# Performance work log

Hardware: AMD Instinct MI355X
Metric: run time of the kernel (lower is better)

The kernel has to match this reference:

```python
import jax, jax.numpy as jnp
import numpy as np

WASHOUT = 200  # matches init kwarg


def setup_inputs() -> dict:
    key = jax.random.key(0)
    k1, k2, k3, k4 = jax.random.split(key, 4)
    N = 4096  # hidden_nodes
    T = 4096  # timeseries length
    density = 0.2  # w_res_density
    u = jax.random.normal(k1, (T,), dtype=jnp.float32)
    # sparse reservoir matrix scaled to spectral radius 0.9
    w_res = jax.random.uniform(k2, (N, N), dtype=jnp.float32) - 0.5
    keep = jax.random.uniform(k3, (N, N)) <= density
    w_res = jnp.where(keep, w_res, 0.0)
    eigs = np.linalg.eigvals(np.asarray(w_res, dtype=np.float64))
    w_res = w_res * jnp.float32(0.9 / np.max(np.abs(eigs)))
    w_in = jax.random.uniform(k4, (N,), dtype=jnp.float32) - 0.5  # uniform distrib, density 1.0, scaling 1.0
    w_out = jnp.ones((N,), dtype=jnp.float32)
    # w_out_density = 1.0 -> mask is a random permutation of all N node indices
    w_out_mask = jax.random.permutation(jax.random.fold_in(key, 7), N).astype(jnp.int32)
    return {"u": u, "w_res": w_res, "w_in": w_in, "w_out": w_out, "w_out_mask": w_out_mask}


def reference(u, w_res, w_in, w_out, w_out_mask):
    N = w_res.shape[0]
    x0 = jnp.zeros((N,), dtype=u.dtype)

    def step(x, u_t):
        x = jnp.tanh(w_in * u_t + w_res @ x)  # [N]
        return x, x[w_out_mask]  # collect masked (permuted) state

    _, X = jax.lax.scan(step, x0, u)  # X: [T, N]
    X = X[WASHOUT:]
    return X @ w_out  # [T - washout]
```

## Files before the change

kernel.cpp:

```cpp
#include <hip/hip_runtime.h>
#include <hip/hip_runtime_api.h>
#include <hip/hip_fp16.h>
#include <math.h>


#define Nn 4096
#define WASHOUT_N 200
#define NBLOCKS 256
#define TPB 1024
#define ROWS_PER_BLOCK 16
#define NWAVES 16
#define ELL_CAP 1024

typedef unsigned long long u64t;
typedef unsigned int u32t;

static __device__ __forceinline__ unsigned short f2h(float f) {
    __half h = __float2half_rn(f);
    union { __half h; unsigned short u; } cv; cv.h = h; return cv.u;
}
static __device__ __forceinline__ float h2f(unsigned short ub) {
    union { __half h; unsigned short u; } cv; cv.u = ub; return __half2float(cv.h);
}

__global__ __launch_bounds__(256) void esn_init(
    const float* __restrict__ w_out, const int* __restrict__ mask,
    u32t* __restrict__ xp_a, u32t* __restrict__ xp_b,
    float* __restrict__ w_eff, float* __restrict__ out, int out_n)
{
    int i = blockIdx.x * blockDim.x + threadIdx.x;
    if (i < Nn) {
        xp_a[i] = 0u;
        xp_b[i] = 0xFFFF0000u;
        w_eff[mask[i]] = w_out[i];
        if (i < out_n) out[i] = 0.0f;
    }
}

__global__ __launch_bounds__(256) void build_ell(
    const float* __restrict__ W, float* __restrict__ ev,
    unsigned short* __restrict__ ec)
{
    int row = blockIdx.x;
    __shared__ unsigned int bank_cnt[32];
    __shared__ unsigned int group_cnt[16];
    if (threadIdx.x < 32) bank_cnt[threadIdx.x] = 0u;
    if (threadIdx.x < 16) group_cnt[threadIdx.x] = 0u;
    __syncthreads();

    const float* wr = W + (size_t)row * Nn;
    size_t base = (size_t)row * ELL_CAP;

    for (int s = threadIdx.x; s < ELL_CAP; s += 256) {
        ev[base + s] = 0.0f;
        ec[base + s] = 0;
    }
    __syncthreads();

    for (int j = threadIdx.x; j < Nn; j += 256) {
        float v = wr[j];
        if (v != 0.0f) {
            unsigned int b  = (unsigned int)j & 31u;
            unsigned int jb = atomicAdd(&bank_cnt[b], 1u);
            unsigned int g  = jb & 15u;
            unsigned int s  = 0xFFFFFFFFu;
            for (int tries = 0; tries < 16; ++tries) {
                unsigned int cand = atomicAdd(&group_cnt[g], 1u);
                if (cand < 64u) { s = cand; break; }
                g = (g + 1u) & 15u;
            }
            if (s != 0xFFFFFFFFu) {
                unsigned int i = g >> 2, k = g & 3u;
                unsigned int pos = 4u * (i * 64u + s) + k;
                ev[base + pos] = v;
                ec[base + pos] = (unsigned short)j;
            }
        }
    }
}

__device__ __forceinline__ u64t xload64(const u64t* p) {
    return __hip_atomic_load(p, __ATOMIC_RELAXED, __HIP_MEMORY_SCOPE_AGENT);
}

__global__ __launch_bounds__(TPB) void esn_step_sparse(
    const float* __restrict__ u, const float* __restrict__ w_in,
    const float* __restrict__ ev, const unsigned short* __restrict__ ec,
    u32t* xp_a, u32t* xp_b, const float* __restrict__ w_eff,
    unsigned short* __restrict__ hist, float* __restrict__ out, int T)
{
    __shared__ __align__(16) float xs[Nn];
    __shared__ u32t  xpub[NWAVES];
    __shared__ float dpart[NWAVES];

    const int tid  = threadIdx.x;
    const int lane = tid & 63;
    const int wave = tid >> 6;
    const int base_row = blockIdx.x * ROWS_PER_BLOCK;
    const int row  = base_row + wave;

    const float wi = w_in[row];
    const float we0 = w_eff[tid];
    const float we1 = w_eff[TPB + tid];
    const float we2 = w_eff[2 * TPB + tid];
    const float we3 = w_eff[3 * TPB + tid];

    const float4*  v4 = (const float4*)(ev + (size_t)row * ELL_CAP);
    const ushort4* c4 = (const ushort4*)(ec + (size_t)row * ELL_CAP);
    const float4  rv0 = v4[lane],       rv1 = v4[64 + lane],
                  rv2 = v4[128 + lane], rv3 = v4[192 + lane];
    const ushort4 rc0 = c4[lane],       rc1 = c4[64 + lane],
                  rc2 = c4[128 + lane], rc3 = c4[192 + lane];

    u32t* bufs[2] = { xp_a, xp_b };
    const bool have_hist = (hist != nullptr);

    for (int t = 0; t <= T; ++t) {
        if (t == T && have_hist) break;

        u32t* xc = bufs[t & 1];
        const u64t tg = (u64t)(u32t)t;
        const float ut = (t < T) ? u[t] : 0.0f;

        const u64t* p = (const u64t*)xc + 2 * tid;
        u64t a = xload64(p);
        u64t b = xload64(p + 1);
        for (;;) {
            bool okA = (((a >> 16) & 0xFFFFull) == tg) && ((a >> 48) == tg);
            bool okB = (((b >> 16) & 0xFFFFull) == tg) && ((b >> 48) == tg);
            if (okA && okB) break;
            __builtin_amdgcn_s_sleep(1);
            if (!okA) a = xload64(p);
            if (!okB) b = xload64(p + 1);
        }
        ((float4*)xs)[tid] = make_float4(
            h2f((unsigned short)(a & 0xFFFF)),
            h2f((unsigned short)((a >> 32) & 0xFFFF)),
            h2f((unsigned short)(b & 0xFFFF)),
            h2f((unsigned short)((b >> 32) & 0xFFFF)));
        __syncthreads();

        if (t < T) {
            float acc = 0.0f;
            acc += rv0.x * xs[rc0.x]; acc += rv0.y * xs[rc0.y];
            acc += rv0.z * xs[rc0.z]; acc += rv0.w * xs[rc0.w];
            acc += rv1.x * xs[rc1.x]; acc += rv1.y * xs[rc1.y];
            acc += rv1.z * xs[rc1.z]; acc += rv1.w * xs[rc1.w];
            acc += rv2.x * xs[rc2.x]; acc += rv2.y * xs[rc2.y];
            acc += rv2.z * xs[rc2.z]; acc += rv2.w * xs[rc2.w];
            acc += rv3.x * xs[rc3.x]; acc += rv3.y * xs[rc3.y];
            acc += rv3.z * xs[rc3.z]; acc += rv3.w * xs[rc3.w];
            #pragma unroll
            for (int off = 32; off > 0; off >>= 1)
                acc += __shfl_xor(acc, off, 64);

            if (lane == 0) {
                float z = __fmaf_rn(wi, ut, acc);
                float e = __expf(2.0f * z);
                float xnew = 1.0f - 2.0f / (e + 1.0f);
                xpub[wave] = ((u32t)(t + 1) << 16) | (u32t)f2h(xnew);
            }
        }

        const bool des = (!have_hist) && (t >= WASHOUT_N + 1) &&
                         ((t & (NBLOCKS - 1)) == (int)blockIdx.x);
        if (des) {
            float d = we0 * xs[tid] + we1 * xs[TPB + tid]
                    + we2 * xs[2 * TPB + tid] + we3 * xs[3 * TPB + tid];
            #pragma unroll
            for (int off = 32; off > 0; off >>= 1)
                d += __shfl_xor(d, off, 64);
            if (lane == 0) dpart[wave] = d;
        }
        __syncthreads();

        if (wave == 0) {
            if (t < T && lane < ROWS_PER_BLOCK) {
                u32t w = xpub[lane];
                __hip_atomic_store(&bufs[(t + 1) & 1][base_row + lane], w,
                                   __ATOMIC_RELAXED, __HIP_MEMORY_SCOPE_AGENT);
                if (have_hist)
                    hist[(size_t)t * Nn + base_row + lane] =
                        (unsigned short)(w & 0xFFFF);
            }
            if (des) {
                float s = (lane < NWAVES) ? dpart[lane] : 0.0f;
                #pragma unroll
                for (int off = 8; off > 0; off >>= 1)
                    s += __shfl_xor(s, off, 64);
                if (lane == 0) out[t - WASHOUT_N - 1] = s;
            }
        }
    }
}

__global__ __launch_bounds__(256) void esn_out_gemv(
    const unsigned short* __restrict__ hist, const float* __restrict__ w_eff,
    float* __restrict__ out, int n_out)
{
    __shared__ float swave[4];
    int k = blockIdx.x;
    if (k >= n_out) return;
    const __half2* hp = (const __half2*)(hist + (size_t)(k + WASHOUT_N) * Nn);
    const int tid = threadIdx.x;
    float acc = 0.0f;
    #pragma unroll
    for (int j = tid; j < Nn / 2; j += 256) {
        float2 xv = __half22float2(hp[j]);
        acc += w_eff[2 * j] * xv.x + w_eff[2 * j + 1] * xv.y;
    }
    #pragma unroll
    for (int off = 32; off > 0; off >>= 1)
        acc += __shfl_xor(acc, off, 64);
    if ((tid & 63) == 0) swave[tid >> 6] = acc;
    __syncthreads();
    if (tid == 0) out[k] = swave[0] + swave[1] + swave[2] + swave[3];
}

extern "C" void kernel_launch(void* const* d_in, const int* in_sizes, int n_in,
                              void* d_out, int out_size, void* d_ws, size_t ws_size,
                              hipStream_t stream)
{
    const float* u     = (const float*)d_in[0];
    const float* W     = (const float*)d_in[1];
    const float* w_in  = (const float*)d_in[2];
    const float* w_out = (const float*)d_in[3];
    const int*   mask  = (const int*)d_in[4];
    float* out = (float*)d_out;
    int T = in_sizes[0];

    const size_t ev_bytes   = (size_t)Nn * ELL_CAP * sizeof(float);
    const size_t ec_bytes   = (size_t)Nn * ELL_CAP * sizeof(unsigned short);
    const size_t hist_bytes = (size_t)Nn * Nn * sizeof(unsigned short);
    const size_t aux_bytes  = 64 * 1024;
    char* ws = (char*)d_ws;

    const bool fits_hist = ws_size >= ev_bytes + ec_bytes + hist_bytes + aux_bytes;
    const bool fits_ell  = ws_size >= ev_bytes + ec_bytes + aux_bytes;

    if (fits_ell) {
        size_t off = ev_bytes + ec_bytes;
        float*          ev    = (float*)(ws);
        unsigned short* ec    = (unsigned short*)(ws + ev_bytes);
        unsigned short* hist  = fits_hist ? (unsigned short*)(ws + off) : nullptr;
        if (fits_hist) off += hist_bytes;
        u32t*           xp_a  = (u32t*)(ws + off);
        u32t*           xp_b  = (u32t*)(ws + off + 16384);
        float*          w_eff = (float*)(ws + off + 32768);

        hipLaunchKernelGGL(esn_init, dim3(16), dim3(256), 0, stream,
                           w_out, mask, xp_a, xp_b, w_eff, out, out_size);
        hipLaunchKernelGGL(build_ell, dim3(Nn), dim3(256), 0, stream, W, ev, ec);

        void* args[] = { (void*)&u, (void*)&w_in, (void*)&ev, (void*)&ec,
                         (void*)&xp_a, (void*)&xp_b, (void*)&w_eff,
                         (void*)&hist, (void*)&out, (void*)&T };
        hipError_t err = hipLaunchCooperativeKernel((const void*)esn_step_sparse,
                                                    dim3(NBLOCKS), dim3(TPB),
                                                    args, 0, stream);
        if (err != hipSuccess) {
            hipLaunchKernelGGL(esn_step_sparse, dim3(NBLOCKS), dim3(TPB), 0, stream,
                               u, w_in, ev, ec, xp_a, xp_b, w_eff, hist, out, T);
        }
        if (fits_hist) {
            hipLaunchKernelGGL(esn_out_gemv, dim3(out_size), dim3(256), 0, stream,
                               hist, w_eff, out, out_size);
        }
    }
}
```

Before: 9.762 ms.

## Double-buffer shared state, publish per wave, trim ELL groups, use DPP reductions

Shared state is double-buffered so the second block-wide barrier per timestep can be removed. Each wave now publishes its own row directly after a DPP-based reduction instead of staging it through shared memory. The ELL builder counts nonzeros per row and packs them into only as many 64-entry groups as needed, so the step kernel can skip unused gather slots. The spin-wait also polls a few times before sleeping. The gains come with more complex synchronisation, and barriers are still taken inside the rarely-true output branch.

```diff
diff --git a/kernel.cpp b/kernel.cpp
--- a/kernel.cpp
+++ b/kernel.cpp
@@ -23,6 +23,10 @@
     union { __half h; unsigned short u; } cv; cv.u = ub; return __half2float(cv.h);
 }
 
+#define DPP_ADD(x, ctrl, rmask)                                              \
+    x += __int_as_float(__builtin_amdgcn_update_dpp(                         \
+        0, __float_as_int(x), (ctrl), (rmask), 0xf, true))
+
 __global__ __launch_bounds__(256) void esn_init(
     const float* __restrict__ w_out, const int* __restrict__ mask,
     u32t* __restrict__ xp_a, u32t* __restrict__ xp_b,
@@ -39,35 +43,47 @@
 
 __global__ __launch_bounds__(256) void build_ell(
     const float* __restrict__ W, float* __restrict__ ev,
-    unsigned short* __restrict__ ec)
+    unsigned short* __restrict__ ec, int* __restrict__ gcnt)
 {
     int row = blockIdx.x;
     __shared__ unsigned int bank_cnt[32];
     __shared__ unsigned int group_cnt[16];
+    __shared__ unsigned int nnz_cnt;
     if (threadIdx.x < 32) bank_cnt[threadIdx.x] = 0u;
     if (threadIdx.x < 16) group_cnt[threadIdx.x] = 0u;
+    if (threadIdx.x == 0) nnz_cnt = 0u;
     __syncthreads();
 
     const float* wr = W + (size_t)row * Nn;
     size_t base = (size_t)row * ELL_CAP;
+
+    unsigned int mycnt = 0;
+    for (int j = threadIdx.x; j < Nn; j += 256)
+        if (wr[j] != 0.0f) ++mycnt;
+    atomicAdd(&nnz_cnt, mycnt);
 
     for (int s = threadIdx.x; s < ELL_CAP; s += 256) {
         ev[base + s] = 0.0f;
         ec[base + s] = 0;
     }
     __syncthreads();
+
+    unsigned int G = (nnz_cnt + 63u) / 64u;
+    if (G < 1u) G = 1u;
+    if (G > 16u) G = 16u;
+    if (threadIdx.x == 0) gcnt[row] = (int)G;
 
     for (int j = threadIdx.x; j < Nn; j += 256) {
         float v = wr[j];
         if (v != 0.0f) {
             unsigned int b  = (unsigned int)j & 31u;
             unsigned int jb = atomicAdd(&bank_cnt[b], 1u);
-            unsigned int g  = jb & 15u;
+            unsigned int g  = jb % G;
             unsigned int s  = 0xFFFFFFFFu;
-            for (int tries = 0; tries < 16; ++tries) {
+            for (unsigned int tries = 0; tries < 16u; ++tries) {
                 unsigned int cand = atomicAdd(&group_cnt[g], 1u);
                 if (cand < 64u) { s = cand; break; }
-                g = (g + 1u) & 15u;
+                g = (g + 1u) % G;
             }
             if (s != 0xFFFFFFFFu) {
                 unsigned int i = g >> 2, k = g & 3u;
@@ -86,11 +102,11 @@
 __global__ __launch_bounds__(TPB) void esn_step_sparse(
     const float* __restrict__ u, const float* __restrict__ w_in,
     const float* __restrict__ ev, const unsigned short* __restrict__ ec,
-    u32t* xp_a, u32t* xp_b, const float* __restrict__ w_eff,
-    unsigned short* __restrict__ hist, float* __restrict__ out, int T)
-{
-    __shared__ __align__(16) float xs[Nn];
-    __shared__ u32t  xpub[NWAVES];
+    const int* __restrict__ gcnt, u32t* xp_a, u32t* xp_b,
+    const float* __restrict__ w_eff, unsigned short* __restrict__ hist,
+    float* __restrict__ out, int T)
+{
+    __shared__ __align__(16) float xs[2][Nn];
     __shared__ float dpart[NWAVES];
 
     const int tid  = threadIdx.x;
@@ -100,6 +116,7 @@
     const int row  = base_row + wave;
 
     const float wi = w_in[row];
+    const int   G  = __builtin_amdgcn_readfirstlane(gcnt[row]);
     const float we0 = w_eff[tid];
     const float we1 = w_eff[TPB + tid];
     const float we2 = w_eff[2 * TPB + tid];
@@ -118,22 +135,24 @@
     for (int t = 0; t <= T; ++t) {
         if (t == T && have_hist) break;
 
-        u32t* xc = bufs[t & 1];
+        u32t* xc  = bufs[t & 1];
+        float* xsp = xs[t & 1];
         const u64t tg = (u64t)(u32t)t;
         const float ut = (t < T) ? u[t] : 0.0f;
 
         const u64t* p = (const u64t*)xc + 2 * tid;
         u64t a = xload64(p);
         u64t b = xload64(p + 1);
+        int spin = 0;
         for (;;) {
             bool okA = (((a >> 16) & 0xFFFFull) == tg) && ((a >> 48) == tg);
             bool okB = (((b >> 16) & 0xFFFFull) == tg) && ((b >> 48) == tg);
             if (okA && okB) break;
-            __builtin_amdgcn_s_sleep(1);
+            if (++spin > 3) __builtin_amdgcn_s_sleep(1);
             if (!okA) a = xload64(p);
             if (!okB) b = xload64(p + 1);
         }
-        ((float4*)xs)[tid] = make_float4(
+        ((float4*)xsp)[tid] = make_float4(
             h2f((unsigned short)(a & 0xFFFF)),
             h2f((unsigned short)((a >> 32) & 0xFFFF)),
             h2f((unsigned short)(b & 0xFFFF)),
@@ -142,53 +161,55 @@
 
         if (t < T) {
             float acc = 0.0f;
-            acc += rv0.x * xs[rc0.x]; acc += rv0.y * xs[rc0.y];
-            acc += rv0.z * xs[rc0.z]; acc += rv0.w * xs[rc0.w];
-            acc += rv1.x * xs[rc1.x]; acc += rv1.y * xs[rc1.y];
-            acc += rv1.z * xs[rc1.z]; acc += rv1.w * xs[rc1.w];
-            acc += rv2.x * xs[rc2.x]; acc += rv2.y * xs[rc2.y];
-            acc += rv2.z * xs[rc2.z]; acc += rv2.w * xs[rc2.w];
-            acc += rv3.x * xs[rc3.x]; acc += rv3.y * xs[rc3.y];
-            acc += rv3.z * xs[rc3.z]; acc += rv3.w * xs[rc3.w];
-            #pragma unroll
-            for (int off = 32; off > 0; off >>= 1)
-                acc += __shfl_xor(acc, off, 64);
-
-            if (lane == 0) {
+            acc += rv0.x * xsp[rc0.x]; acc += rv0.y * xsp[rc0.y];
+            acc += rv0.z * xsp[rc0.z]; acc += rv0.w * xsp[rc0.w];
+            acc += rv1.x * xsp[rc1.x]; acc += rv1.y * xsp[rc1.y];
+            acc += rv1.z * xsp[rc1.z]; acc += rv1.w * xsp[rc1.w];
+            acc += rv2.x * xsp[rc2.x]; acc += rv2.y * xsp[rc2.y];
+            acc += rv2.z * xsp[rc2.z]; acc += rv2.w * xsp[rc2.w];
+            if (G > 12) acc += rv3.x * xsp[rc3.x];
+            if (G > 13) acc += rv3.y * xsp[rc3.y];
+            if (G > 14) acc += rv3.z * xsp[rc3.z];
+            if (G > 15) acc += rv3.w * xsp[rc3.w];
+
+            DPP_ADD(acc, 0x111, 0xf);
+            DPP_ADD(acc, 0x112, 0xf);
+            DPP_ADD(acc, 0x114, 0xf);
+            DPP_ADD(acc, 0x118, 0xf);
+            DPP_ADD(acc, 0x142, 0xa);
+            DPP_ADD(acc, 0x143, 0xc);
+
+            if (lane == 63) {
                 float z = __fmaf_rn(wi, ut, acc);
                 float e = __expf(2.0f * z);
                 float xnew = 1.0f - 2.0f / (e + 1.0f);
-                xpub[wave] = ((u32t)(t + 1) << 16) | (u32t)f2h(xnew);
-            }
-        }
-
-        const bool des = (!have_hist) && (t >= WASHOUT_N + 1) &&
-                         ((t & (NBLOCKS - 1)) == (int)blockIdx.x);
-        if (des) {
-            float d = we0 * xs[tid] + we1 * xs[TPB + tid]
-                    + we2 * xs[2 * TPB + tid] + we3 * xs[3 * TPB + tid];
-            #pragma unroll
-            for (int off = 32; off > 0; off >>= 1)
-                d += __shfl_xor(d, off, 64);
-            if (lane == 0) dpart[wave] = d;
-        }
-        __syncthreads();
-
-        if (wave == 0) {
-            if (t < T && lane < ROWS_PER_BLOCK) {
-                u32t w = xpub[lane];
-                __hip_atomic_store(&bufs[(t + 1) & 1][base_row + lane], w,
+                u32t w = ((u32t)(t + 1) << 16) | (u32t)f2h(xnew);
+                __hip_atomic_store(&bufs[(t + 1) & 1][row], w,
                                    __ATOMIC_RELAXED, __HIP_MEMORY_SCOPE_AGENT);
                 if (have_hist)
-                    hist[(size_t)t * Nn + base_row + lane] =
-                        (unsigned short)(w & 0xFFFF);
-            }
+                    hist[(size_t)t * Nn + row] = (unsigned short)(w & 0xFFFF);
+            }
+        }
+
+        if (!have_hist) {
+            const bool des = (t >= WASHOUT_N + 1) &&
+                             ((t & (NBLOCKS - 1)) == (int)blockIdx.x);
             if (des) {
-                float s = (lane < NWAVES) ? dpart[lane] : 0.0f;
+                float d = we0 * xsp[tid] + we1 * xsp[TPB + tid]
+                        + we2 * xsp[2 * TPB + tid] + we3 * xsp[3 * TPB + tid];
                 #pragma unroll
-                for (int off = 8; off > 0; off >>= 1)
-                    s += __shfl_xor(s, off, 64);
-                if (lane == 0) out[t - WASHOUT_N - 1] = s;
+                for (int off = 32; off > 0; off >>= 1)
+                    d += __shfl_xor(d, off, 64);
+                if (lane == 0) dpart[wave] = d;
+                __syncthreads();
+                if (wave == 0) {
+                    float s = (lane < NWAVES) ? dpart[lane] : 0.0f;
+                    #pragma unroll
+                    for (int off = 8; off > 0; off >>= 1)
+                        s += __shfl_xor(s, off, 64);
+                    if (lane == 0) out[t - WASHOUT_N - 1] = s;
+                }
+                __syncthreads();
             }
         }
     }
@@ -231,36 +252,41 @@
 
     const size_t ev_bytes   = (size_t)Nn * ELL_CAP * sizeof(float);
     const size_t ec_bytes   = (size_t)Nn * ELL_CAP * sizeof(unsigned short);
+    const size_t gc_bytes   = (size_t)Nn * sizeof(int);
     const size_t hist_bytes = (size_t)Nn * Nn * sizeof(unsigned short);
     const size_t aux_bytes  = 64 * 1024;
     char* ws = (char*)d_ws;
 
-    const bool fits_hist = ws_size >= ev_bytes + ec_bytes + hist_bytes + aux_bytes;
-    const bool fits_ell  = ws_size >= ev_bytes + ec_bytes + aux_bytes;
+    const bool fits_hist =
+        ws_size >= ev_bytes + ec_bytes + gc_bytes + hist_bytes + aux_bytes;
+    const bool fits_ell = ws_size >= ev_bytes + ec_bytes + gc_bytes + aux_bytes;
 
     if (fits_ell) {
-        size_t off = ev_bytes + ec_bytes;
-        float*          ev    = (float*)(ws);
-        unsigned short* ec    = (unsigned short*)(ws + ev_bytes);
-        unsigned short* hist  = fits_hist ? (unsigned short*)(ws + off) : nullptr;
-        if (fits_hist) off += hist_bytes;
+        size_t off = 0;
+        float*          ev    = (float*)(ws + off);  off += ev_bytes;
+        unsigned short* ec    = (unsigned short*)(ws + off);  off += ec_bytes;
+        int*            gcnt  = (int*)(ws + off);  off += gc_bytes;
+        unsigned short* hist  = nullptr;
+        if (fits_hist) { hist = (unsigned short*)(ws + off); off += hist_bytes; }
         u32t*           xp_a  = (u32t*)(ws + off);
         u32t*           xp_b  = (u32t*)(ws + off + 16384);
         float*          w_eff = (float*)(ws + off + 32768);
 
         hipLaunchKernelGGL(esn_init, dim3(16), dim3(256), 0, stream,
                            w_out, mask, xp_a, xp_b, w_eff, out, out_size);
-        hipLaunchKernelGGL(build_ell, dim3(Nn), dim3(256), 0, stream, W, ev, ec);
+        hipLaunchKernelGGL(build_ell, dim3(Nn), dim3(256), 0, stream,
+                           W, ev, ec, gcnt);
 
         void* args[] = { (void*)&u, (void*)&w_in, (void*)&ev, (void*)&ec,
-                         (void*)&xp_a, (void*)&xp_b, (void*)&w_eff,
-                         (void*)&hist, (void*)&out, (void*)&T };
+                         (void*)&gcnt, (void*)&xp_a, (void*)&xp_b,
+                         (void*)&w_eff, (void*)&hist, (void*)&out, (void*)&T };
         hipError_t err = hipLaunchCooperativeKernel((const void*)esn_step_sparse,
                                                     dim3(NBLOCKS), dim3(TPB),
                                                     args, 0, stream);
         if (err != hipSuccess) {
             hipLaunchKernelGGL(esn_step_sparse, dim3(NBLOCKS), dim3(TPB), 0, stream,
-                               u, w_in, ev, ec, xp_a, xp_b, w_eff, hist, out, T);
+                               u, w_in, ev, ec, gcnt, xp_a, xp_b, w_eff, hist,
+                               out, T);
         }
         if (fits_hist) {
             hipLaunchKernelGGL(esn_out_gemv, dim3(out_size), dim3(256), 0, stream,
```

After: 31.00 ms. 3.18x slower.

## Split each reservoir row across two waves and double the block count

Applied to the files above, without the earlier changes.

Each row's sparse dot product is now split over two waves, each handling half of the ELL entries. Partial sums meet in shared memory, and wave 0 applies tanh and publishes the value. With 8 rows per block, the grid grows to 512 blocks so more CUs share the per-step work and each wave's serial gather chain is shorter. The cost is more blocks polling the shared state buffer each step, a second reduction stage, and a cooperative launch that now has to fit two 1024-thread blocks per CU.

```diff
diff --git a/kernel.cpp b/kernel.cpp
--- a/kernel.cpp
+++ b/kernel.cpp
@@ -6,9 +6,9 @@
 
 #define Nn 4096
 #define WASHOUT_N 200
-#define NBLOCKS 256
+#define NBLOCKS 512
 #define TPB 1024
-#define ROWS_PER_BLOCK 16
+#define ROWS_PER_BLOCK 8
 #define NWAVES 16
 #define ELL_CAP 1024
 
@@ -83,23 +83,24 @@
     return __hip_atomic_load(p, __ATOMIC_RELAXED, __HIP_MEMORY_SCOPE_AGENT);
 }
 
-__global__ __launch_bounds__(TPB) void esn_step_sparse(
+__global__ __launch_bounds__(TPB, 8) void esn_step_sparse(
     const float* __restrict__ u, const float* __restrict__ w_in,
     const float* __restrict__ ev, const unsigned short* __restrict__ ec,
     u32t* xp_a, u32t* xp_b, const float* __restrict__ w_eff,
     unsigned short* __restrict__ hist, float* __restrict__ out, int T)
 {
     __shared__ __align__(16) float xs[Nn];
-    __shared__ u32t  xpub[NWAVES];
+    __shared__ float hpart[NWAVES];
     __shared__ float dpart[NWAVES];
 
     const int tid  = threadIdx.x;
     const int lane = tid & 63;
     const int wave = tid >> 6;
     const int base_row = blockIdx.x * ROWS_PER_BLOCK;
-    const int row  = base_row + wave;
-
-    const float wi = w_in[row];
+    const int row  = base_row + (wave >> 1);
+    const int half = wave & 1;
+
+    const float wi_pub = (lane < ROWS_PER_BLOCK) ? w_in[base_row + lane] : 0.0f;
     const float we0 = w_eff[tid];
     const float we1 = w_eff[TPB + tid];
     const float we2 = w_eff[2 * TPB + tid];
@@ -107,10 +108,9 @@
 
     const float4*  v4 = (const float4*)(ev + (size_t)row * ELL_CAP);
     const ushort4* c4 = (const ushort4*)(ec + (size_t)row * ELL_CAP);
-    const float4  rv0 = v4[lane],       rv1 = v4[64 + lane],
-                  rv2 = v4[128 + lane], rv3 = v4[192 + lane];
-    const ushort4 rc0 = c4[lane],       rc1 = c4[64 + lane],
-                  rc2 = c4[128 + lane], rc3 = c4[192 + lane];
+    const int i0 = half * 2, i1 = half * 2 + 1;
+    const float4  rv0 = v4[i0 * 64 + lane], rv1 = v4[i1 * 64 + lane];
+    const ushort4 rc0 = c4[i0 * 64 + lane], rc1 = c4[i1 * 64 + lane];
 
     u32t* bufs[2] = { xp_a, xp_b };
     const bool have_hist = (hist != nullptr);
@@ -146,20 +146,10 @@
             acc += rv0.z * xs[rc0.z]; acc += rv0.w * xs[rc0.w];
             acc += rv1.x * xs[rc1.x]; acc += rv1.y * xs[rc1.y];
             acc += rv1.z * xs[rc1.z]; acc += rv1.w * xs[rc1.w];
-            acc += rv2.x * xs[rc2.x]; acc += rv2.y * xs[rc2.y];
-            acc += rv2.z * xs[rc2.z]; acc += rv2.w * xs[rc2.w];
-            acc += rv3.x * xs[rc3.x]; acc += rv3.y * xs[rc3.y];
-            acc += rv3.z * xs[rc3.z]; acc += rv3.w * xs[rc3.w];
             #pragma unroll
             for (int off = 32; off > 0; off >>= 1)
                 acc += __shfl_xor(acc, off, 64);
-
-            if (lane == 0) {
-                float z = __fmaf_rn(wi, ut, acc);
-                float e = __expf(2.0f * z);
-                float xnew = 1.0f - 2.0f / (e + 1.0f);
-                xpub[wave] = ((u32t)(t + 1) << 16) | (u32t)f2h(xnew);
-            }
+            if (lane == 0) hpart[wave] = acc;
         }
 
         const bool des = (!have_hist) && (t >= WASHOUT_N + 1) &&
@@ -176,7 +166,11 @@
 
         if (wave == 0) {
             if (t < T && lane < ROWS_PER_BLOCK) {
-                u32t w = xpub[lane];
+                float s = hpart[2 * lane] + hpart[2 * lane + 1];
+                float z = __fmaf_rn(wi_pub, ut, s);
+                float e = __expf(2.0f * z);
+                float xnew = 1.0f - 2.0f / (e + 1.0f);
+                u32t w = ((u32t)(t + 1) << 16) | (u32t)f2h(xnew);
                 __hip_atomic_store(&bufs[(t + 1) & 1][base_row + lane], w,
                                    __ATOMIC_RELAXED, __HIP_MEMORY_SCOPE_AGENT);
                 if (have_hist)
@@ -235,15 +229,16 @@
     const size_t aux_bytes  = 64 * 1024;
     char* ws = (char*)d_ws;
 
-    const bool fits_hist = ws_size >= ev_bytes + ec_bytes + hist_bytes + aux_bytes;
-    const bool fits_ell  = ws_size >= ev_bytes + ec_bytes + aux_bytes;
+    const bool fits_hist =
+        ws_size >= ev_bytes + ec_bytes + hist_bytes + aux_bytes;
+    const bool fits_ell = ws_size >= ev_bytes + ec_bytes + aux_bytes;
 
     if (fits_ell) {
-        size_t off = ev_bytes + ec_bytes;
-        float*          ev    = (float*)(ws);
-        unsigned short* ec    = (unsigned short*)(ws + ev_bytes);
-        unsigned short* hist  = fits_hist ? (unsigned short*)(ws + off) : nullptr;
-        if (fits_hist) off += hist_bytes;
+        size_t off = 0;
+        float*          ev    = (float*)(ws + off);  off += ev_bytes;
+        unsigned short* ec    = (unsigned short*)(ws + off);  off += ec_bytes;
+        unsigned short* hist  = nullptr;
+        if (fits_hist) { hist = (unsigned short*)(ws + off); off += hist_bytes; }
         u32t*           xp_a  = (u32t*)(ws + off);
         u32t*           xp_b  = (u32t*)(ws + off + 16384);
         float*          w_eff = (float*)(ws + off + 32768);
```

New measurement: 19.57 ms. 2.01x slower.
